# Performance work log

Measured on AMD Instinct MI355X. Metric: run time of the kernel, lower is better.

The kernel has to match this reference:

```python
import jax, jax.numpy as jnp
import numpy as np

DECAY = 0.99
EPS = 1e-12  # torch F.normalize eps


def setup_inputs() -> dict:
    key = jax.random.key(0)
    ks = jax.random.split(key, 5)
    B, S, H, M = 4, 4096, 1024, 256
    x = jax.random.normal(ks[0], (B, S, H), dtype=jnp.float32)
    Wq = jax.random.normal(ks[1], (M, H), dtype=jnp.float32) * (H ** -0.5)
    Wk = jax.random.normal(ks[2], (M, H), dtype=jnp.float32) * (H ** -0.5)
    Wv = jax.random.normal(ks[3], (M, H), dtype=jnp.float32) * (H ** -0.5)
    # original inits W_out to zeros; use small random weights so the baseline output is non-trivial
    Wo = jax.random.normal(ks[4], (H, M), dtype=jnp.float32) * (M ** -0.5)
    M0 = jnp.zeros((M, M), dtype=jnp.float32)
    return {"x": x, "Wq": Wq, "Wk": Wk, "Wv": Wv, "Wo": Wo, "M0": M0, "chunk_size": 64}


def _l2norm(t):
    return t / jnp.maximum(jnp.linalg.norm(t, axis=-1, keepdims=True), EPS)


def reference(x, Wq, Wk, Wv, Wo, M0, chunk_size):
    B, S, H = x.shape
    m = Wq.shape[0]
    q = jnp.einsum('bsh,mh->bsm', x, Wq)
    k = _l2norm(jnp.einsum('bsh,mh->bsm', x, Wk))
    v = _l2norm(jnp.einsum('bsh,mh->bsm', x, Wv))
    n_chunks = S // chunk_size
    # (n_chunks, B, c, m)
    qc = q.reshape(B, n_chunks, chunk_size, m).transpose(1, 0, 2, 3)
    kc = k.reshape(B, n_chunks, chunk_size, m).transpose(1, 0, 2, 3)
    vc = v.reshape(B, n_chunks, chunk_size, m).transpose(1, 0, 2, 3)
    decay_c = DECAY ** chunk_size
    scale = 1.0 / (B * chunk_size)

    def step(M, qkv):
        qch, kch, vch = qkv
        r = jnp.einsum('bcm,nm->bcn', qch, M)  # q @ M.T
        outer = jnp.einsum('bci,bcj->ij', vch, kch) * scale
        return decay_c * M + outer, r

    _, rs = jax.lax.scan(step, M0, (qc, kc, vc))  # rs: (n_chunks, B, c, m)
    retrieved = rs.transpose(1, 0, 2, 3).reshape(B, S, m)
    return jnp.einsum('bsm,hm->bsh', retrieved, Wo)
```

## Files before the change

### kernel.cpp

```cpp
#include <hip/hip_runtime.h>
#include <math.h>

#define BB 4
#define SS 4096
#define HH 1024
#define MM 256
#define CHUNK 64
#define NCHUNK 64
#define ROWS (BB*SS)
#define QKV_LD 768
#define DECAY_F 0.99

typedef unsigned short u16;
typedef __attribute__((ext_vector_type(8))) short bf16x8;
typedef __attribute__((ext_vector_type(8))) unsigned short u16x8;
typedef __attribute__((ext_vector_type(4))) float f32x4;

__device__ inline u16 f2b(float f) {
  union { float f; unsigned u; } v; v.f = f;
  unsigned r = v.u + 0x7FFF + ((v.u >> 16) & 1);
  return (u16)(r >> 16);
}
__device__ inline float b2f(u16 h) {
  union { unsigned u; float f; } v; v.u = ((unsigned)h) << 16; return v.f;
}

__device__ inline void gload16(const void* g, void* l) {
  __builtin_amdgcn_global_load_lds(
      (const __attribute__((address_space(1))) unsigned int*)g,
      (__attribute__((address_space(3))) unsigned int*)l, 16, 0, 0);
}

__global__ __launch_bounds__(256) void cast_x_kernel(const float* __restrict__ src,
                                                     u16* __restrict__ dst) {
  int i = blockIdx.x * 256 + threadIdx.x;
  float4 v = reinterpret_cast<const float4*>(src)[i];
  ushort4 o;
  o.x = f2b(v.x); o.y = f2b(v.y); o.z = f2b(v.z); o.w = f2b(v.w);
  reinterpret_cast<ushort4*>(dst)[i] = o;
}

__global__ __launch_bounds__(256) void cast_w_kernel(const float* __restrict__ Wq,
                                                     const float* __restrict__ Wk,
                                                     const float* __restrict__ Wv,
                                                     const float* __restrict__ Wo,
                                                     u16* __restrict__ Wqkv_b,
                                                     u16* __restrict__ Wo_b) {
  int b = blockIdx.x, which = b >> 8;
  int i = ((b & 255) << 8) + threadIdx.x;
  const float* src = which == 0 ? Wq : which == 1 ? Wk : which == 2 ? Wv : Wo;
  u16* dst = which < 3 ? Wqkv_b + which * (MM * HH) : Wo_b;
  float4 v = reinterpret_cast<const float4*>(src)[i];
  ushort4 o;
  o.x = f2b(v.x); o.y = f2b(v.y); o.z = f2b(v.z); o.w = f2b(v.w);
  reinterpret_cast<ushort4*>(dst)[i] = o;
}

#define M_STD_BF16 0
#define M_STD_F32  1
#define M_OUTER    2
#define M_RETR     3

template<int MODE>
__global__ __launch_bounds__(256) void gemm128(const u16* __restrict__ A,
                                               const u16* __restrict__ Bg,
                                               const float* __restrict__ Bf,
                                               void* __restrict__ Cv,
                                               int K, int lda, int ldb, int ldc,
                                               float scale) {
  __shared__ bf16x8 As[512];
  __shared__ bf16x8 Bs[512];
  const int tid = threadIdx.x, lane = tid & 63, wv = tid >> 6;
  const int wr = wv >> 1, wc = wv & 1;
  const int t = (MODE == M_OUTER || MODE == M_RETR) ? blockIdx.z : 0;
  const int row0 = blockIdx.y * 128;
  const int col0 = blockIdx.x * 128;
  const int NK = K >> 5;
  const float* Mt = (MODE == M_RETR) ? (Bf + (size_t)t * (MM * MM)) : nullptr;

  auto stage = [&](int ks) {
    int koff;
    if (MODE == M_OUTER) koff = ((ks >> 1) << 12) + t * CHUNK + ((ks & 1) << 5);
    else                 koff = ks << 5;
#pragma unroll
    for (int j = 0; j < 2; ++j) {
      int m = j * 4 + wv;
      int rf = m * 16 + (lane & 15);
      size_t arow;
      if (MODE == M_RETR)
        arow = (size_t)(2 * blockIdx.y + (rf >> 6)) * SS + (size_t)t * CHUNK + (rf & 63);
      else
        arow = (size_t)(row0 + rf);
      const u16* ga = A + arow * (size_t)lda + koff + ((lane >> 4) << 3);
      gload16(ga, &As[m * 64]);
      if (MODE != M_RETR) {
        const u16* gb = Bg + (size_t)(col0 + rf) * ldb + koff + ((lane >> 4) << 3);
        gload16(gb, &Bs[m * 64]);
      }
    }
    if (MODE == M_RETR) {
#pragma unroll
      for (int j = 0; j < 2; ++j) {
        int s = tid + j * 256;
        int n = (s >> 6) * 16 + (lane & 15);
        const float* gm = Mt + (size_t)(col0 + n) * MM + (ks << 5) + ((lane >> 4) << 3);
        float4 f0 = *reinterpret_cast<const float4*>(gm);
        float4 f1 = *reinterpret_cast<const float4*>(gm + 4);
        u16x8 h;
        h[0] = f2b(f0.x); h[1] = f2b(f0.y); h[2] = f2b(f0.z); h[3] = f2b(f0.w);
        h[4] = f2b(f1.x); h[5] = f2b(f1.y); h[6] = f2b(f1.z); h[7] = f2b(f1.w);
        *reinterpret_cast<u16x8*>(&Bs[s]) = h;
      }
    }
  };

  f32x4 acc[4][4] = {};
  stage(0);
  for (int ks = 0; ks < NK; ++ks) {
    __syncthreads();
    bf16x8 af[4], bfr[4];
#pragma unroll
    for (int m = 0; m < 4; ++m) af[m] = As[(wr * 4 + m) * 64 + lane];
#pragma unroll
    for (int n = 0; n < 4; ++n) bfr[n] = Bs[(wc * 4 + n) * 64 + lane];
#pragma unroll
    for (int m = 0; m < 4; ++m)
#pragma unroll
      for (int n = 0; n < 4; ++n)
        acc[m][n] = __builtin_amdgcn_mfma_f32_16x16x32_bf16(af[m], bfr[n], acc[m][n], 0, 0, 0);
    if (ks + 1 < NK) {
      __syncthreads();
      stage(ks + 1);
    }
  }

  const int r4 = (lane >> 4) << 2;
  const int cc = lane & 15;
#pragma unroll
  for (int m = 0; m < 4; ++m)
#pragma unroll
    for (int n = 0; n < 4; ++n)
#pragma unroll
      for (int r = 0; r < 4; ++r) {
        int lr = wr * 64 + m * 16 + r4 + r;
        int lc = wc * 64 + n * 16 + cc;
        float vv = acc[m][n][r];
        if (MODE == M_STD_BF16) {
          ((u16*)Cv)[(size_t)(row0 + lr) * ldc + col0 + lc] = f2b(vv);
        } else if (MODE == M_STD_F32) {
          ((float*)Cv)[(size_t)(row0 + lr) * ldc + col0 + lc] = vv;
        } else if (MODE == M_OUTER) {
          ((float*)Cv)[(size_t)t * (MM * MM) + (size_t)(row0 + lr) * MM + col0 + lc] = vv * scale;
        } else {
          size_t rowg = (size_t)(2 * blockIdx.y + (lr >> 6)) * SS + (size_t)t * CHUNK + (lr & 63);
          ((u16*)Cv)[rowg * MM + col0 + lc] = f2b(vv);
        }
      }
}

__global__ __launch_bounds__(256) void l2normT_kernel(const u16* __restrict__ qkv,
                                                      u16* __restrict__ kT,
                                                      u16* __restrict__ vT) {
  __shared__ u16 T[256][72];
  __shared__ float ps[64][4];
  __shared__ float inv[64];
  const int tid = threadIdx.x;
  const int q = tid >> 6, rl = tid & 63;
  const int row0 = blockIdx.x * 64;
#pragma unroll 1
  for (int seg = 0; seg < 2; ++seg) {
    u16* dstT = seg ? vT : kT;
    const int segbase = 256 + seg * 256;
    float ss = 0.f;
#pragma unroll
    for (int i = 0; i < 8; ++i) {
      u16x8 v = *reinterpret_cast<const u16x8*>(
          qkv + (size_t)(row0 + rl) * QKV_LD + segbase + q * 64 + i * 8);
#pragma unroll
      for (int e = 0; e < 8; ++e) {
        float f = b2f(v[e]);
        ss += f * f;
        T[q * 64 + i * 8 + e][rl] = v[e];
      }
    }
    ps[rl][q] = ss;
    __syncthreads();
    if (tid < 64) {
      float s = ps[tid][0] + ps[tid][1] + ps[tid][2] + ps[tid][3];
      inv[tid] = 1.0f / fmaxf(sqrtf(s), 1e-12f);
    }
    __syncthreads();
#pragma unroll
    for (int p = 0; p < 8; ++p) {
      int c = p * 32 + q * 8 + (rl >> 3);
      int r0 = (rl & 7) * 8;
      u16x8 val = *reinterpret_cast<const u16x8*>(&T[c][r0]);
      u16x8 o;
#pragma unroll
      for (int e = 0; e < 8; ++e) o[e] = f2b(b2f(val[e]) * inv[r0 + e]);
      *reinterpret_cast<u16x8*>(dstT + (size_t)c * ROWS + row0 + r0) = o;
    }
    __syncthreads();
  }
}

__global__ __launch_bounds__(256) void prefix_kernel(float* __restrict__ outer,
                                                     const float* __restrict__ M0,
                                                     float decay_c) {
  int ij = blockIdx.x * 256 + threadIdx.x;
  float run = M0[ij];
  float pre[8];
#pragma unroll
  for (int d = 0; d < 8; ++d) pre[d] = outer[(size_t)d * (MM * MM) + ij];
#pragma unroll 1
  for (int tb = 0; tb < NCHUNK; tb += 8) {
#pragma unroll
    for (int d = 0; d < 8; ++d) {
      int tc = tb + d;
      float o = pre[d];
      if (tb + 8 < NCHUNK) pre[d] = outer[(size_t)(tc + 8) * (MM * MM) + ij];
      outer[(size_t)tc * (MM * MM) + ij] = run;
      run = decay_c * run + o;
    }
  }
}

extern "C" void kernel_launch(void* const* d_in, const int* in_sizes, int n_in,
                              void* d_out, int out_size, void* d_ws, size_t ws_size,
                              hipStream_t stream) {
  const float* x  = (const float*)d_in[0];
  const float* Wq = (const float*)d_in[1];
  const float* Wk = (const float*)d_in[2];
  const float* Wv = (const float*)d_in[3];
  const float* Wo = (const float*)d_in[4];
  const float* M0 = (const float*)d_in[5];
  float* out = (float*)d_out;

  char* ws = (char*)d_ws;
  u16*   xb     = (u16*)(ws);
  u16*   qkv_b  = (u16*)(ws + 33554432);
  u16*   Wqkv_b = (u16*)(ws + 58720256);
  u16*   Wo_b   = (u16*)(ws + 60293120);
  u16*   kT     = (u16*)(ws);
  u16*   vT     = (u16*)(ws + 8388608);
  float* outer  = (float*)(ws + 16777216);
  u16*   r_b    = (u16*)(ws);

  const float scale   = 1.0f / (BB * CHUNK);
  const float decay_c = (float)pow(DECAY_F, (double)CHUNK);
  dim3 blk(256);

  cast_x_kernel<<<(ROWS * HH / 4) / 256, blk, 0, stream>>>(x, xb);
  cast_w_kernel<<<1024, blk, 0, stream>>>(Wq, Wk, Wv, Wo, Wqkv_b, Wo_b);
  gemm128<M_STD_BF16><<<dim3(QKV_LD / 128, ROWS / 128), blk, 0, stream>>>(
      xb, Wqkv_b, nullptr, qkv_b, HH, HH, HH, QKV_LD, 0.f);
  l2normT_kernel<<<ROWS / 64, blk, 0, stream>>>(qkv_b, kT, vT);
  gemm128<M_OUTER><<<dim3(2, 2, NCHUNK), blk, 0, stream>>>(
      vT, kT, nullptr, outer, MM, ROWS, ROWS, MM, scale);
  prefix_kernel<<<(MM * MM) / 256, blk, 0, stream>>>(outer, M0, decay_c);
  gemm128<M_RETR><<<dim3(2, 2, NCHUNK), blk, 0, stream>>>(
      qkv_b, nullptr, outer, r_b, MM, QKV_LD, 0, MM, 0.f);
  gemm128<M_STD_F32><<<dim3(HH / 128, ROWS / 128), blk, 0, stream>>>(
      r_b, Wo_b, nullptr, out, MM, MM, MM, HH, 0.f);
}
```

Baseline: 158.9 us.

## Double-buffer LDS tiles in gemm128 and remap workgroups across XCDs

Adds double-buffered LDS tiles so the next K-step's global loads are issued before the current step's MFMAs, leaving one barrier per iteration instead of two. For the standard GEMM modes it also remaps linear workgroup IDs so consecutive tiles land on the same XCD chiplet, which should improve L2 reuse. The cost is twice the LDS per block, which may lower occupancy. The remap assumes the grid size is divisible by 8.

```diff
diff --git a/kernel.cpp b/kernel.cpp
--- a/kernel.cpp
+++ b/kernel.cpp
@@ -68,17 +68,28 @@
                                                void* __restrict__ Cv,
                                                int K, int lda, int ldb, int ldc,
                                                float scale) {
-  __shared__ bf16x8 As[512];
-  __shared__ bf16x8 Bs[512];
+  __shared__ bf16x8 As[2][512];
+  __shared__ bf16x8 Bs[2][512];
   const int tid = threadIdx.x, lane = tid & 63, wv = tid >> 6;
   const int wr = wv >> 1, wc = wv & 1;
   const int t = (MODE == M_OUTER || MODE == M_RETR) ? blockIdx.z : 0;
-  const int row0 = blockIdx.y * 128;
-  const int col0 = blockIdx.x * 128;
+
+  int bx, by;
+  if (MODE == M_STD_BF16 || MODE == M_STD_F32) {
+    int gx = gridDim.x;
+    int nwg = gx * gridDim.y;
+    int lin = blockIdx.y * gx + blockIdx.x;
+    int chunk = nwg >> 3;
+    int orig = (lin & 7) * chunk + (lin >> 3);
+    bx = orig % gx; by = orig / gx;
+  } else { bx = blockIdx.x; by = blockIdx.y; }
+
+  const int row0 = by * 128;
+  const int col0 = bx * 128;
   const int NK = K >> 5;
   const float* Mt = (MODE == M_RETR) ? (Bf + (size_t)t * (MM * MM)) : nullptr;
 
-  auto stage = [&](int ks) {
+  auto stage = [&](int ks, int buf) {
     int koff;
     if (MODE == M_OUTER) koff = ((ks >> 1) << 12) + t * CHUNK + ((ks & 1) << 5);
     else                 koff = ks << 5;
@@ -88,14 +99,14 @@
       int rf = m * 16 + (lane & 15);
       size_t arow;
       if (MODE == M_RETR)
-        arow = (size_t)(2 * blockIdx.y + (rf >> 6)) * SS + (size_t)t * CHUNK + (rf & 63);
+        arow = (size_t)(2 * by + (rf >> 6)) * SS + (size_t)t * CHUNK + (rf & 63);
       else
         arow = (size_t)(row0 + rf);
       const u16* ga = A + arow * (size_t)lda + koff + ((lane >> 4) << 3);
-      gload16(ga, &As[m * 64]);
+      gload16(ga, &As[buf][m * 64]);
       if (MODE != M_RETR) {
         const u16* gb = Bg + (size_t)(col0 + rf) * ldb + koff + ((lane >> 4) << 3);
-        gload16(gb, &Bs[m * 64]);
+        gload16(gb, &Bs[buf][m * 64]);
       }
     }
     if (MODE == M_RETR) {
@@ -109,29 +120,27 @@
         u16x8 h;
         h[0] = f2b(f0.x); h[1] = f2b(f0.y); h[2] = f2b(f0.z); h[3] = f2b(f0.w);
         h[4] = f2b(f1.x); h[5] = f2b(f1.y); h[6] = f2b(f1.z); h[7] = f2b(f1.w);
-        *reinterpret_cast<u16x8*>(&Bs[s]) = h;
+        *reinterpret_cast<u16x8*>(&Bs[buf][s]) = h;
       }
     }
   };
 
   f32x4 acc[4][4] = {};
-  stage(0);
+  stage(0, 0);
   for (int ks = 0; ks < NK; ++ks) {
     __syncthreads();
+    if (ks + 1 < NK) stage(ks + 1, (ks + 1) & 1);
+    const int buf = ks & 1;
     bf16x8 af[4], bfr[4];
 #pragma unroll
-    for (int m = 0; m < 4; ++m) af[m] = As[(wr * 4 + m) * 64 + lane];
-#pragma unroll
-    for (int n = 0; n < 4; ++n) bfr[n] = Bs[(wc * 4 + n) * 64 + lane];
+    for (int m = 0; m < 4; ++m) af[m] = As[buf][(wr * 4 + m) * 64 + lane];
+#pragma unroll
+    for (int n = 0; n < 4; ++n) bfr[n] = Bs[buf][(wc * 4 + n) * 64 + lane];
 #pragma unroll
     for (int m = 0; m < 4; ++m)
 #pragma unroll
       for (int n = 0; n < 4; ++n)
         acc[m][n] = __builtin_amdgcn_mfma_f32_16x16x32_bf16(af[m], bfr[n], acc[m][n], 0, 0, 0);
-    if (ks + 1 < NK) {
-      __syncthreads();
-      stage(ks + 1);
-    }
   }
 
   const int r4 = (lane >> 4) << 2;
@@ -152,7 +161,7 @@
         } else if (MODE == M_OUTER) {
           ((float*)Cv)[(size_t)t * (MM * MM) + (size_t)(row0 + lr) * MM + col0 + lc] = vv * scale;
         } else {
-          size_t rowg = (size_t)(2 * blockIdx.y + (lr >> 6)) * SS + (size_t)t * CHUNK + (lr & 63);
+          size_t rowg = (size_t)(2 * by + (lr >> 6)) * SS + (size_t)t * CHUNK + (lr & 63);
           ((u16*)Cv)[rowg * MM + col0 + lc] = f2b(vv);
         }
       }
```

New measurement: 157.1 us. About the same (-1.1%).
